# Kernel tuning notes

Measured on AMD Instinct MI355X. Metric: run time of the kernel, lower is better.

Reference implementation:

```python
import jax, jax.numpy as jnp
import numpy as np

LEAKY_ALPHA = 0.2  # TF default for tf.nn.leaky_relu


def setup_inputs() -> dict:
    key = jax.random.key(0)
    ks = jax.random.split(key, 5)
    B, N, F, O, H = 2, 4096, 256, 64, 4
    x = jax.random.normal(ks[0], (B, N, F), dtype=jnp.float32)
    bias = jax.random.normal(ks[1], (B, N, N), dtype=jnp.float32)
    W = jax.random.normal(ks[2], (H, F, O), dtype=jnp.float32) * (1.0 / np.sqrt(F))
    a = jax.random.normal(ks[3], (H, O), dtype=jnp.float32) * (1.0 / np.sqrt(O))
    b = jax.random.normal(ks[4], (H, O), dtype=jnp.float32) * 0.01
    return {"x": x, "bias": bias, "W": W, "a": a, "b": b}


def reference(x, bias, W, a, b):
    # x: [B,N,F], bias: [B,N,N], W: [H,F,O], a: [H,O], b: [H,O]
    h = jnp.einsum('bnf,hfo->bhno', x, W)          # transformed inputs per head
    w = jnp.einsum('bhno,ho->bhn', h, a)           # scalar score per node
    scores = w[:, :, :, None] + w[:, :, None, :]   # [B,H,N,N]: w_i + w_j
    logits = jax.nn.leaky_relu(scores, LEAKY_ALPHA) + bias[:, None, :, :]
    coefs = jax.nn.softmax(logits, axis=3)
    heads = jnp.einsum('bhnm,bhmo->bhno', coefs, h) + b[None, :, None, :]
    return jnp.mean(heads, axis=1)                 # (1/H) * sum of heads -> [B,N,O]
```

## Files before the change

### kernel.cpp

```cpp
#include <hip/hip_runtime.h>
#include <hip/hip_bf16.h>


constexpr int Bc = 2, Nc = 4096, Fc = 256, Oc = 64, Hc = 4;
constexpr float ALPHA = 0.2f;
constexpr float LOG2E = 1.4426950408889634f;

constexpr int BSTR = 260;
constexpr int BBUF = 16 * BSTR;
constexpr int SMEMF = 2 * BBUF;
constexpr int SLOTF = 1088;

typedef __attribute__((ext_vector_type(8))) short bf16x8;
typedef __attribute__((ext_vector_type(4))) float f32x4;

static __device__ inline short f2bf(float x) {
    __hip_bfloat16 h = __float2bfloat16(x);
    return *reinterpret_cast<short*>(&h);
}

static __device__ inline unsigned int rnpack(float a, float b) {
    const unsigned int au = __float_as_uint(a) + 0x8000u;
    const unsigned int bu = __float_as_uint(b) + 0x8000u;
    return (au >> 16) | (bu & 0xffff0000u);
}

static __device__ inline int frag_off(int jt, int k, int lane, int t) {
    return jt * 4096 + k * 512 + lane * 8 + t;
}

static __device__ inline void bar_lgkm() {
    asm volatile("s_waitcnt lgkmcnt(0)" ::: "memory");
    __builtin_amdgcn_s_barrier();
}

__global__ __launch_bounds__(256) void k_h(const float* __restrict__ x,
                                           const float* __restrict__ W,
                                           const float* __restrict__ a,
                                           short* __restrict__ hTB,
                                           float* __restrict__ wout) {
    __shared__ float xs[64][132];
    const int nb = Nc / 64;
    const int blk = blockIdx.x;
    const int nt = blk % nb;
    const int bh = blk / nb;
    const int h = bh % Hc;
    const int b = bh / Hc;
    const int tid = threadIdx.x;
    const int o_id = tid & 15, n_id = tid >> 4;
    const int o0 = o_id * 4, n0 = n_id * 4;

    float acc[4][4] = {};

    for (int fs = 0; fs < Fc; fs += 128) {
#pragma unroll
        for (int it = 0; it < 8; ++it) {
            int idx = it * 256 + tid;
            int r = idx >> 5, c = idx & 31;
            const float4 v = *reinterpret_cast<const float4*>(
                &x[((size_t)(b * Nc + nt * 64 + r)) * Fc + fs + c * 4]);
            *reinterpret_cast<float4*>(&xs[r][c * 4]) = v;
        }
        __syncthreads();
        for (int f = 0; f < 128; ++f) {
            const float4 wv = *reinterpret_cast<const float4*>(
                &W[((size_t)(h * Fc + fs + f)) * Oc + o0]);
            float xv[4];
#pragma unroll
            for (int r = 0; r < 4; ++r) xv[r] = xs[n0 + r][f];
#pragma unroll
            for (int r = 0; r < 4; ++r) {
                acc[r][0] = __builtin_fmaf(xv[r], wv.x, acc[r][0]);
                acc[r][1] = __builtin_fmaf(xv[r], wv.y, acc[r][1]);
                acc[r][2] = __builtin_fmaf(xv[r], wv.z, acc[r][2]);
                acc[r][3] = __builtin_fmaf(xv[r], wv.w, acc[r][3]);
            }
        }
        __syncthreads();
    }

    const float4 av = *reinterpret_cast<const float4*>(&a[h * Oc + o0]);
    float part[4];
#pragma unroll
    for (int r = 0; r < 4; ++r) {
        part[r] = acc[r][0] * av.x + acc[r][1] * av.y + acc[r][2] * av.z +
                  acc[r][3] * av.w;
#pragma unroll
        for (int off = 1; off < 16; off <<= 1)
            part[r] += __shfl_xor(part[r], off, 64);
    }
    const int n_glob = nt * 64 + n0;
    if (o_id == 0) {
#pragma unroll
        for (int r = 0; r < 4; ++r)
            wout[((size_t)(b * Hc + h)) * Nc + n_glob + r] = part[r] * LOG2E;
    }
    const int sub = n0 >> 5;
    const int lg = (n0 >> 3) & 3;
    const int t0 = n0 & 7;
    short* base = hTB + ((size_t)(b * Hc + h)) * (Nc * Oc);
#pragma unroll
    for (int c = 0; c < 4; ++c) {
        const int o = o0 + c;
        const int of = o >> 4, li = o & 15;
        short4 v;
        v.x = f2bf(acc[0][c]);
        v.y = f2bf(acc[1][c]);
        v.z = f2bf(acc[2][c]);
        v.w = f2bf(acc[3][c]);
        *reinterpret_cast<short4*>(&base[frag_off(nt, of * 2 + sub, lg * 16 + li, t0)]) = v;
    }
}

__global__ __launch_bounds__(512, 2) void k_attn(
    const float* __restrict__ bias, const float* __restrict__ wrowL,
    const short* __restrict__ hTB, float* __restrict__ hps) {
    __shared__ float smem[SMEMF];

    const int blk = blockIdx.x;
    const int xcd = blk & 7;
    const int lin = blk >> 3;
    const int pair = lin & 1;
    const int tl = xcd * 64 + (lin >> 1);
    const int it = tl & 255;
    const int b = tl >> 8;
    const int i0 = it * 16;
    const int tid = threadIdx.x;
    const int w = tid >> 6;
    const int hd = pair * 2 + (w & 1);
    const int q = w >> 1;
    const int lane = tid & 63;
    const int li = lane & 15, lg = lane >> 4;
    const int jl0 = lg * 8;

    const float wiL = wrowL[((size_t)(b * Hc + hd)) * Nc + i0 + li];
    const float* __restrict__ wjb = &wrowL[((size_t)(b * Hc + hd)) * Nc];
    const short* __restrict__ fb =
        hTB + ((size_t)(b * Hc + hd)) * (Nc * Oc) + lane * 8;

    const int srow = tid >> 5, sc4 = (tid & 31) * 4;
    const float* __restrict__ ssrc =
        &bias[((size_t)(b * Nc + i0 + srow)) * Nc + sc4];
    float* const sdst = &smem[srow * BSTR + sc4];

    f32x4 acc[4] = {{0.f, 0.f, 0.f, 0.f},
                    {0.f, 0.f, 0.f, 0.f},
                    {0.f, 0.f, 0.f, 0.f},
                    {0.f, 0.f, 0.f, 0.f}};
    float l_run = 0.f;

    {
        const float4 t0 = *reinterpret_cast<const float4*>(ssrc);
        const float4 t1 = *reinterpret_cast<const float4*>(ssrc + 128);
        *reinterpret_cast<float4*>(sdst) = t0;
        *reinterpret_cast<float4*>(sdst + 128) = t1;
    }
    float4 pA0 = *reinterpret_cast<const float4*>(ssrc + 256);
    float4 pA1 = *reinterpret_cast<const float4*>(ssrc + 256 + 128);
    bar_lgkm();

#pragma unroll 1
    for (int st = 0; st < 16; ++st) {
        if (st + 1 < 16) {
            float* d = sdst + ((st + 1) & 1) * BBUF;
            *reinterpret_cast<float4*>(d) = pA0;
            *reinterpret_cast<float4*>(d + 128) = pA1;
        }
        if (st + 2 < 16) {
            const float* sp = ssrc + (size_t)(st + 2) * 256;
            pA0 = *reinterpret_cast<const float4*>(sp);
            pA1 = *reinterpret_cast<const float4*>(sp + 128);
        }

        const int jt = st * 4 + q;
        bf16x8 fr[8];
#pragma unroll
        for (int k = 0; k < 8; ++k)
            fr[k] = *reinterpret_cast<const bf16x8*>(fb + jt * 4096 + k * 512);
        const int j0 = st * 256 + q * 64;
        const float* bp = &smem[(st & 1) * BBUF + li * BSTR + q * 64 + jl0];
        const float4 b03 = *reinterpret_cast<const float4*>(bp);
        const float4 b47 = *reinterpret_cast<const float4*>(bp + 4);
        const float4 b8b = *reinterpret_cast<const float4*>(bp + 32);
        const float4 bcf = *reinterpret_cast<const float4*>(bp + 36);
        const float bb[16] = {b03.x, b03.y, b03.z, b03.w, b47.x, b47.y,
                              b47.z, b47.w, b8b.x, b8b.y, b8b.z, b8b.w,
                              bcf.x, bcf.y, bcf.z, bcf.w};
        float s[16];
#pragma unroll
        for (int u = 0; u < 4; ++u) {
            const int off = (u >> 1) * 32 + (u & 1) * 4;
            const float4 wv =
                *reinterpret_cast<const float4*>(&wjb[j0 + jl0 + off]);
            float v, lv;
            v = wiL + wv.x; lv = fmaxf(v, ALPHA * v);
            s[u * 4 + 0] = __builtin_amdgcn_exp2f(__builtin_fmaf(bb[u * 4 + 0], LOG2E, lv));
            v = wiL + wv.y; lv = fmaxf(v, ALPHA * v);
            s[u * 4 + 1] = __builtin_amdgcn_exp2f(__builtin_fmaf(bb[u * 4 + 1], LOG2E, lv));
            v = wiL + wv.z; lv = fmaxf(v, ALPHA * v);
            s[u * 4 + 2] = __builtin_amdgcn_exp2f(__builtin_fmaf(bb[u * 4 + 2], LOG2E, lv));
            v = wiL + wv.w; lv = fmaxf(v, ALPHA * v);
            s[u * 4 + 3] = __builtin_amdgcn_exp2f(__builtin_fmaf(bb[u * 4 + 3], LOG2E, lv));
        }
        const float ta = (s[0] + s[1]) + (s[2] + s[3]);
        const float tb = (s[4] + s[5]) + (s[6] + s[7]);
        const float tc = (s[8] + s[9]) + (s[10] + s[11]);
        const float td = (s[12] + s[13]) + (s[14] + s[15]);
        l_run += (ta + tb) + (tc + td);
        bf16x8 pa0, pa1;
        unsigned int* pw0 = reinterpret_cast<unsigned int*>(&pa0);
        unsigned int* pw1 = reinterpret_cast<unsigned int*>(&pa1);
#pragma unroll
        for (int k2 = 0; k2 < 4; ++k2) {
            pw0[k2] = rnpack(s[k2 * 2], s[k2 * 2 + 1]);
            pw1[k2] = rnpack(s[8 + k2 * 2], s[8 + k2 * 2 + 1]);
        }
        __builtin_amdgcn_s_setprio(1);
#pragma unroll
        for (int of = 0; of < 4; ++of) {
            acc[of] = __builtin_amdgcn_mfma_f32_16x16x32_bf16(pa0, fr[of * 2 + 0],
                                                              acc[of], 0, 0, 0);
            acc[of] = __builtin_amdgcn_mfma_f32_16x16x32_bf16(pa1, fr[of * 2 + 1],
                                                              acc[of], 0, 0, 0);
        }
        __builtin_amdgcn_s_setprio(0);
        bar_lgkm();
    }

    if (q) {
        float* base = smem + ((w & 1) * 3 + (q - 1)) * SLOTF;
#pragma unroll
        for (int of = 0; of < 4; ++of)
            *reinterpret_cast<f32x4*>(&base[of * 256 + lane * 4]) = acc[of];
        base[1024 + lane] = l_run;
    }
    __syncthreads();
    if (q == 0) {
#pragma unroll
        for (int s = 0; s < 3; ++s) {
            const float* base = smem + ((w & 1) * 3 + s) * SLOTF;
#pragma unroll
            for (int of = 0; of < 4; ++of) {
                const f32x4 p =
                    *reinterpret_cast<const f32x4*>(&base[of * 256 + lane * 4]);
                acc[of][0] += p[0];
                acc[of][1] += p[1];
                acc[of][2] += p[2];
                acc[of][3] += p[3];
            }
            l_run += base[1024 + lane];
        }
        float lrow = l_run + __shfl_xor(l_run, 16, 64);
        lrow += __shfl_xor(lrow, 32, 64);
        const float linv = 1.0f / lrow;
        float sc[4];
#pragma unroll
        for (int r = 0; r < 4; ++r) sc[r] = __shfl(linv, lg * 4 + r, 64);
        float* hp = hps + (((size_t)(b * Hc + hd)) * Nc + i0) * Oc;
#pragma unroll
        for (int of = 0; of < 4; ++of)
#pragma unroll
            for (int r = 0; r < 4; ++r)
                hp[(size_t)(lg * 4 + r) * Oc + of * 16 + li] = acc[of][r] * sc[r];
    }
}

__global__ __launch_bounds__(256) void k_out(const float* __restrict__ hps,
                                             const float* __restrict__ bvec,
                                             float* __restrict__ out) {
    const int e = blockIdx.x * 256 + threadIdx.x;
    const int col = e & 63;
    const int bn = e >> 6;
    const int b = bn >> 12;
    const size_t plane = (size_t)Nc * Oc;
    const size_t off = ((size_t)(b * Hc) * Nc + (bn & 4095)) * Oc + col;
    const float v = hps[off] + hps[off + plane] + hps[off + 2 * plane] +
                    hps[off + 3 * plane];
    const float bm = 0.25f * (bvec[col] + bvec[Oc + col] + bvec[2 * Oc + col] +
                              bvec[3 * Oc + col]);
    out[e] = 0.25f * v + bm;
}

extern "C" void kernel_launch(void* const* d_in, const int* in_sizes, int n_in,
                              void* d_out, int out_size, void* d_ws, size_t ws_size,
                              hipStream_t stream) {
    const float* x = (const float*)d_in[0];
    const float* bias = (const float*)d_in[1];
    const float* W = (const float*)d_in[2];
    const float* a = (const float*)d_in[3];
    const float* bvec = (const float*)d_in[4];
    float* out = (float*)d_out;

    char* ws = (char*)d_ws;
    short* hTB = (short*)ws;
    float* wbuf = (float*)(ws + (size_t)Bc * Hc * Oc * Nc * 2);
    float* hps = (float*)(ws + (size_t)Bc * Hc * Oc * Nc * 2 +
                          (size_t)Bc * Hc * Nc * 4);

    k_h<<<Bc * Hc * (Nc / 64), 256, 0, stream>>>(x, W, a, hTB, wbuf);
    k_attn<<<Bc * (Nc / 16) * (Hc / 2), 512, 0, stream>>>(bias, wbuf, hTB, hps);
    k_out<<<(Bc * Nc * Oc) / 256, 256, 0, stream>>>(hps, bvec, out);
}
```

Before: 98.24 us.

## Process all four heads per block and fuse head-mean output into attention kernel

Each attention block now covers all four heads for its 16-row tile, with two waves per head each handling half of the key chunks, in place of two heads split four ways. This halves the grid and means each block loads its bias tile once for all four heads instead of twice across two blocks. The per-head results are reduced in shared memory and averaged with the bias vector directly into the output, which removes the hps intermediate buffer and the separate k_out launch. The trade-off is fewer blocks (512) and more serial work per wave, which may reduce latency hiding.

```diff
diff --git a/kernel.cpp b/kernel.cpp
--- a/kernel.cpp
+++ b/kernel.cpp
@@ -114,21 +114,21 @@
 
 __global__ __launch_bounds__(512, 2) void k_attn(
     const float* __restrict__ bias, const float* __restrict__ wrowL,
-    const short* __restrict__ hTB, float* __restrict__ hps) {
+    const short* __restrict__ hTB, const float* __restrict__ bvec,
+    float* __restrict__ out) {
     __shared__ float smem[SMEMF];
 
     const int blk = blockIdx.x;
     const int xcd = blk & 7;
     const int lin = blk >> 3;
-    const int pair = lin & 1;
-    const int tl = xcd * 64 + (lin >> 1);
+    const int tl = xcd * 64 + lin;
     const int it = tl & 255;
     const int b = tl >> 8;
     const int i0 = it * 16;
     const int tid = threadIdx.x;
     const int w = tid >> 6;
-    const int hd = pair * 2 + (w & 1);
-    const int q = w >> 1;
+    const int hd = w & 3;
+    const int half = w >> 2;
     const int lane = tid & 63;
     const int li = lane & 15, lg = lane >> 4;
     const int jl0 = lg * 8;
@@ -172,113 +172,115 @@
             pA1 = *reinterpret_cast<const float4*>(sp + 128);
         }
 
-        const int jt = st * 4 + q;
-        bf16x8 fr[8];
-#pragma unroll
-        for (int k = 0; k < 8; ++k)
-            fr[k] = *reinterpret_cast<const bf16x8*>(fb + jt * 4096 + k * 512);
-        const int j0 = st * 256 + q * 64;
-        const float* bp = &smem[(st & 1) * BBUF + li * BSTR + q * 64 + jl0];
-        const float4 b03 = *reinterpret_cast<const float4*>(bp);
-        const float4 b47 = *reinterpret_cast<const float4*>(bp + 4);
-        const float4 b8b = *reinterpret_cast<const float4*>(bp + 32);
-        const float4 bcf = *reinterpret_cast<const float4*>(bp + 36);
-        const float bb[16] = {b03.x, b03.y, b03.z, b03.w, b47.x, b47.y,
-                              b47.z, b47.w, b8b.x, b8b.y, b8b.z, b8b.w,
-                              bcf.x, bcf.y, bcf.z, bcf.w};
-        float s[16];
-#pragma unroll
-        for (int u = 0; u < 4; ++u) {
-            const int off = (u >> 1) * 32 + (u & 1) * 4;
-            const float4 wv =
-                *reinterpret_cast<const float4*>(&wjb[j0 + jl0 + off]);
-            float v, lv;
-            v = wiL + wv.x; lv = fmaxf(v, ALPHA * v);
-            s[u * 4 + 0] = __builtin_amdgcn_exp2f(__builtin_fmaf(bb[u * 4 + 0], LOG2E, lv));
-            v = wiL + wv.y; lv = fmaxf(v, ALPHA * v);
-            s[u * 4 + 1] = __builtin_amdgcn_exp2f(__builtin_fmaf(bb[u * 4 + 1], LOG2E, lv));
-            v = wiL + wv.z; lv = fmaxf(v, ALPHA * v);
-            s[u * 4 + 2] = __builtin_amdgcn_exp2f(__builtin_fmaf(bb[u * 4 + 2], LOG2E, lv));
-            v = wiL + wv.w; lv = fmaxf(v, ALPHA * v);
-            s[u * 4 + 3] = __builtin_amdgcn_exp2f(__builtin_fmaf(bb[u * 4 + 3], LOG2E, lv));
-        }
-        const float ta = (s[0] + s[1]) + (s[2] + s[3]);
-        const float tb = (s[4] + s[5]) + (s[6] + s[7]);
-        const float tc = (s[8] + s[9]) + (s[10] + s[11]);
-        const float td = (s[12] + s[13]) + (s[14] + s[15]);
-        l_run += (ta + tb) + (tc + td);
-        bf16x8 pa0, pa1;
-        unsigned int* pw0 = reinterpret_cast<unsigned int*>(&pa0);
-        unsigned int* pw1 = reinterpret_cast<unsigned int*>(&pa1);
-#pragma unroll
-        for (int k2 = 0; k2 < 4; ++k2) {
-            pw0[k2] = rnpack(s[k2 * 2], s[k2 * 2 + 1]);
-            pw1[k2] = rnpack(s[8 + k2 * 2], s[8 + k2 * 2 + 1]);
-        }
-        __builtin_amdgcn_s_setprio(1);
-#pragma unroll
-        for (int of = 0; of < 4; ++of) {
-            acc[of] = __builtin_amdgcn_mfma_f32_16x16x32_bf16(pa0, fr[of * 2 + 0],
-                                                              acc[of], 0, 0, 0);
-            acc[of] = __builtin_amdgcn_mfma_f32_16x16x32_bf16(pa1, fr[of * 2 + 1],
-                                                              acc[of], 0, 0, 0);
-        }
-        __builtin_amdgcn_s_setprio(0);
+#pragma unroll
+        for (int c = 0; c < 2; ++c) {
+            const int jc = half * 2 + c;
+            const int jt = st * 4 + jc;
+            const int j0 = st * 256 + jc * 64;
+            bf16x8 fr[8];
+#pragma unroll
+            for (int k = 0; k < 8; ++k)
+                fr[k] = *reinterpret_cast<const bf16x8*>(fb + jt * 4096 + k * 512);
+            const float* bp = &smem[(st & 1) * BBUF + li * BSTR + jc * 64 + jl0];
+            const float4 b03 = *reinterpret_cast<const float4*>(bp);
+            const float4 b47 = *reinterpret_cast<const float4*>(bp + 4);
+            const float4 b8b = *reinterpret_cast<const float4*>(bp + 32);
+            const float4 bcf = *reinterpret_cast<const float4*>(bp + 36);
+            const float bb[16] = {b03.x, b03.y, b03.z, b03.w, b47.x, b47.y,
+                                  b47.z, b47.w, b8b.x, b8b.y, b8b.z, b8b.w,
+                                  bcf.x, bcf.y, bcf.z, bcf.w};
+            float s[16];
+#pragma unroll
+            for (int u = 0; u < 4; ++u) {
+                const int off = (u >> 1) * 32 + (u & 1) * 4;
+                const float4 wv =
+                    *reinterpret_cast<const float4*>(&wjb[j0 + jl0 + off]);
+                float v, lv;
+                v = wiL + wv.x; lv = fmaxf(v, ALPHA * v);
+                s[u * 4 + 0] = __builtin_amdgcn_exp2f(__builtin_fmaf(bb[u * 4 + 0], LOG2E, lv));
+                v = wiL + wv.y; lv = fmaxf(v, ALPHA * v);
+                s[u * 4 + 1] = __builtin_amdgcn_exp2f(__builtin_fmaf(bb[u * 4 + 1], LOG2E, lv));
+                v = wiL + wv.z; lv = fmaxf(v, ALPHA * v);
+                s[u * 4 + 2] = __builtin_amdgcn_exp2f(__builtin_fmaf(bb[u * 4 + 2], LOG2E, lv));
+                v = wiL + wv.w; lv = fmaxf(v, ALPHA * v);
+                s[u * 4 + 3] = __builtin_amdgcn_exp2f(__builtin_fmaf(bb[u * 4 + 3], LOG2E, lv));
+            }
+            const float ta = (s[0] + s[1]) + (s[2] + s[3]);
+            const float tb = (s[4] + s[5]) + (s[6] + s[7]);
+            const float tc = (s[8] + s[9]) + (s[10] + s[11]);
+            const float td = (s[12] + s[13]) + (s[14] + s[15]);
+            l_run += (ta + tb) + (tc + td);
+            bf16x8 pa0, pa1;
+            unsigned int* pw0 = reinterpret_cast<unsigned int*>(&pa0);
+            unsigned int* pw1 = reinterpret_cast<unsigned int*>(&pa1);
+#pragma unroll
+            for (int k2 = 0; k2 < 4; ++k2) {
+                pw0[k2] = rnpack(s[k2 * 2], s[k2 * 2 + 1]);
+                pw1[k2] = rnpack(s[8 + k2 * 2], s[8 + k2 * 2 + 1]);
+            }
+            __builtin_amdgcn_s_setprio(1);
+#pragma unroll
+            for (int of = 0; of < 4; ++of) {
+                acc[of] = __builtin_amdgcn_mfma_f32_16x16x32_bf16(
+                    pa0, fr[of * 2 + 0], acc[of], 0, 0, 0);
+                acc[of] = __builtin_amdgcn_mfma_f32_16x16x32_bf16(
+                    pa1, fr[of * 2 + 1], acc[of], 0, 0, 0);
+            }
+            __builtin_amdgcn_s_setprio(0);
+        }
         bar_lgkm();
     }
 
-    if (q) {
-        float* base = smem + ((w & 1) * 3 + (q - 1)) * SLOTF;
+    if (half) {
+        float* base = smem + hd * SLOTF;
 #pragma unroll
         for (int of = 0; of < 4; ++of)
             *reinterpret_cast<f32x4*>(&base[of * 256 + lane * 4]) = acc[of];
         base[1024 + lane] = l_run;
     }
     __syncthreads();
-    if (q == 0) {
-#pragma unroll
-        for (int s = 0; s < 3; ++s) {
-            const float* base = smem + ((w & 1) * 3 + s) * SLOTF;
-#pragma unroll
-            for (int of = 0; of < 4; ++of) {
-                const f32x4 p =
-                    *reinterpret_cast<const f32x4*>(&base[of * 256 + lane * 4]);
-                acc[of][0] += p[0];
-                acc[of][1] += p[1];
-                acc[of][2] += p[2];
-                acc[of][3] += p[3];
-            }
-            l_run += base[1024 + lane];
-        }
+    if (!half) {
+        float* base = smem + hd * SLOTF;
+#pragma unroll
+        for (int of = 0; of < 4; ++of) {
+            const f32x4 p =
+                *reinterpret_cast<const f32x4*>(&base[of * 256 + lane * 4]);
+            acc[of][0] += p[0];
+            acc[of][1] += p[1];
+            acc[of][2] += p[2];
+            acc[of][3] += p[3];
+        }
+        l_run += base[1024 + lane];
         float lrow = l_run + __shfl_xor(l_run, 16, 64);
         lrow += __shfl_xor(lrow, 32, 64);
         const float linv = 1.0f / lrow;
         float sc[4];
 #pragma unroll
         for (int r = 0; r < 4; ++r) sc[r] = __shfl(linv, lg * 4 + r, 64);
-        float* hp = hps + (((size_t)(b * Hc + hd)) * Nc + i0) * Oc;
-#pragma unroll
-        for (int of = 0; of < 4; ++of)
-#pragma unroll
-            for (int r = 0; r < 4; ++r)
-                hp[(size_t)(lg * 4 + r) * Oc + of * 16 + li] = acc[of][r] * sc[r];
-    }
-}
-
-__global__ __launch_bounds__(256) void k_out(const float* __restrict__ hps,
-                                             const float* __restrict__ bvec,
-                                             float* __restrict__ out) {
-    const int e = blockIdx.x * 256 + threadIdx.x;
-    const int col = e & 63;
-    const int bn = e >> 6;
-    const int b = bn >> 12;
-    const size_t plane = (size_t)Nc * Oc;
-    const size_t off = ((size_t)(b * Hc) * Nc + (bn & 4095)) * Oc + col;
-    const float v = hps[off] + hps[off + plane] + hps[off + 2 * plane] +
-                    hps[off + 3 * plane];
-    const float bm = 0.25f * (bvec[col] + bvec[Oc + col] + bvec[2 * Oc + col] +
-                              bvec[3 * Oc + col]);
-    out[e] = 0.25f * v + bm;
+#pragma unroll
+        for (int of = 0; of < 4; ++of) {
+            f32x4 nv;
+            nv[0] = acc[of][0] * sc[0];
+            nv[1] = acc[of][1] * sc[1];
+            nv[2] = acc[of][2] * sc[2];
+            nv[3] = acc[of][3] * sc[3];
+            *reinterpret_cast<f32x4*>(&base[of * 256 + lane * 4]) = nv;
+        }
+    }
+    __syncthreads();
+#pragma unroll
+    for (int k = 0; k < 2; ++k) {
+        const int e = k * 512 + tid;
+        const int row = e >> 6, col = e & 63;
+        const int ofo = col >> 4, lio = col & 15, lgo = row >> 2, ro = row & 3;
+        const int eoff = ofo * 256 + (lgo * 16 + lio) * 4 + ro;
+        float osum = 0.f;
+#pragma unroll
+        for (int h = 0; h < 4; ++h) osum += smem[h * SLOTF + eoff];
+        const float bm = 0.25f * (bvec[col] + bvec[Oc + col] +
+                                  bvec[2 * Oc + col] + bvec[3 * Oc + col]);
+        out[((size_t)(b * Nc + i0 + row)) * Oc + col] = 0.25f * osum + bm;
+    }
 }
 
 extern "C" void kernel_launch(void* const* d_in, const int* in_sizes, int n_in,
@@ -294,10 +296,7 @@
     char* ws = (char*)d_ws;
     short* hTB = (short*)ws;
     float* wbuf = (float*)(ws + (size_t)Bc * Hc * Oc * Nc * 2);
-    float* hps = (float*)(ws + (size_t)Bc * Hc * Oc * Nc * 2 +
-                          (size_t)Bc * Hc * Nc * 4);
 
     k_h<<<Bc * Hc * (Nc / 64), 256, 0, stream>>>(x, W, a, hTB, wbuf);
-    k_attn<<<Bc * (Nc / 16) * (Hc / 2), 512, 0, stream>>>(bias, wbuf, hTB, hps);
-    k_out<<<(Bc * Nc * Oc) / 256, 256, 0, stream>>>(hps, bvec, out);
-}
+    k_attn<<<Bc * (Nc / 16), 512, 0, stream>>>(bias, wbuf, hTB, bvec, out);
+}
```

New measurement: 102.6 us. 4.5% more time.

## Split attention output columns across two wave groups with 1024-thread blocks

Applied to the files above, without the earlier changes.

Doubles the attention block to 1024 threads and splits the 64 output columns between two halves of the waves, so each wave holds two accumulators and loads four B fragments instead of eight. The bias tile staging is spread over more threads, with one float4 per thread per stage. This lowers per-wave register use so more waves can hide latency. The cost is that the softmax exponentials and score computation are now done twice, once in each output half, and there is more reduction traffic through shared memory. The launch bound of 1024 threads with 8 blocks is also an aggressive occupancy request.

```diff
diff --git a/kernel.cpp b/kernel.cpp
--- a/kernel.cpp
+++ b/kernel.cpp
@@ -9,7 +9,7 @@
 constexpr int BSTR = 260;
 constexpr int BBUF = 16 * BSTR;
 constexpr int SMEMF = 2 * BBUF;
-constexpr int SLOTF = 1088;
+constexpr int PSLOT = 576;
 
 typedef __attribute__((ext_vector_type(8))) short bf16x8;
 typedef __attribute__((ext_vector_type(4))) float f32x4;
@@ -112,7 +112,7 @@
     }
 }
 
-__global__ __launch_bounds__(512, 2) void k_attn(
+__global__ __launch_bounds__(1024, 8) void k_attn(
     const float* __restrict__ bias, const float* __restrict__ wrowL,
     const short* __restrict__ hTB, float* __restrict__ hps) {
     __shared__ float smem[SMEMF];
@@ -128,7 +128,8 @@
     const int tid = threadIdx.x;
     const int w = tid >> 6;
     const int hd = pair * 2 + (w & 1);
-    const int q = w >> 1;
+    const int q = (w >> 1) & 3;
+    const int oh = w >> 3;
     const int lane = tid & 63;
     const int li = lane & 15, lg = lane >> 4;
     const int jl0 = lg * 8;
@@ -136,47 +137,34 @@
     const float wiL = wrowL[((size_t)(b * Hc + hd)) * Nc + i0 + li];
     const float* __restrict__ wjb = &wrowL[((size_t)(b * Hc + hd)) * Nc];
     const short* __restrict__ fb =
-        hTB + ((size_t)(b * Hc + hd)) * (Nc * Oc) + lane * 8;
-
-    const int srow = tid >> 5, sc4 = (tid & 31) * 4;
+        hTB + ((size_t)(b * Hc + hd)) * (Nc * Oc) + oh * 4 * 512 + lane * 8;
+
+    const int srow = tid >> 6, sc4 = tid & 63;
     const float* __restrict__ ssrc =
-        &bias[((size_t)(b * Nc + i0 + srow)) * Nc + sc4];
-    float* const sdst = &smem[srow * BSTR + sc4];
-
-    f32x4 acc[4] = {{0.f, 0.f, 0.f, 0.f},
-                    {0.f, 0.f, 0.f, 0.f},
-                    {0.f, 0.f, 0.f, 0.f},
-                    {0.f, 0.f, 0.f, 0.f}};
+        &bias[((size_t)(b * Nc + i0 + srow)) * Nc + sc4 * 4];
+    float* const sdst = &smem[srow * BSTR + sc4 * 4];
+
+    f32x4 acc0 = {0.f, 0.f, 0.f, 0.f};
+    f32x4 acc1 = {0.f, 0.f, 0.f, 0.f};
     float l_run = 0.f;
 
-    {
-        const float4 t0 = *reinterpret_cast<const float4*>(ssrc);
-        const float4 t1 = *reinterpret_cast<const float4*>(ssrc + 128);
-        *reinterpret_cast<float4*>(sdst) = t0;
-        *reinterpret_cast<float4*>(sdst + 128) = t1;
-    }
-    float4 pA0 = *reinterpret_cast<const float4*>(ssrc + 256);
-    float4 pA1 = *reinterpret_cast<const float4*>(ssrc + 256 + 128);
+    *reinterpret_cast<float4*>(sdst) = *reinterpret_cast<const float4*>(ssrc);
+    float4 pA = *reinterpret_cast<const float4*>(ssrc + 256);
     bar_lgkm();
 
 #pragma unroll 1
     for (int st = 0; st < 16; ++st) {
-        if (st + 1 < 16) {
-            float* d = sdst + ((st + 1) & 1) * BBUF;
-            *reinterpret_cast<float4*>(d) = pA0;
-            *reinterpret_cast<float4*>(d + 128) = pA1;
-        }
-        if (st + 2 < 16) {
-            const float* sp = ssrc + (size_t)(st + 2) * 256;
-            pA0 = *reinterpret_cast<const float4*>(sp);
-            pA1 = *reinterpret_cast<const float4*>(sp + 128);
-        }
+        if (st + 1 < 16)
+            *reinterpret_cast<float4*>(sdst + ((st + 1) & 1) * BBUF) = pA;
+        if (st + 2 < 16)
+            pA = *reinterpret_cast<const float4*>(ssrc + (size_t)(st + 2) * 256);
 
         const int jt = st * 4 + q;
-        bf16x8 fr[8];
-#pragma unroll
-        for (int k = 0; k < 8; ++k)
-            fr[k] = *reinterpret_cast<const bf16x8*>(fb + jt * 4096 + k * 512);
+        const short* fp = fb + jt * 4096;
+        const bf16x8 fr0 = *reinterpret_cast<const bf16x8*>(fp);
+        const bf16x8 fr1 = *reinterpret_cast<const bf16x8*>(fp + 512);
+        const bf16x8 fr2 = *reinterpret_cast<const bf16x8*>(fp + 1024);
+        const bf16x8 fr3 = *reinterpret_cast<const bf16x8*>(fp + 1536);
         const int j0 = st * 256 + q * 64;
         const float* bp = &smem[(st & 1) * BBUF + li * BSTR + q * 64 + jl0];
         const float4 b03 = *reinterpret_cast<const float4*>(bp);
@@ -216,39 +204,34 @@
             pw1[k2] = rnpack(s[8 + k2 * 2], s[8 + k2 * 2 + 1]);
         }
         __builtin_amdgcn_s_setprio(1);
-#pragma unroll
-        for (int of = 0; of < 4; ++of) {
-            acc[of] = __builtin_amdgcn_mfma_f32_16x16x32_bf16(pa0, fr[of * 2 + 0],
-                                                              acc[of], 0, 0, 0);
-            acc[of] = __builtin_amdgcn_mfma_f32_16x16x32_bf16(pa1, fr[of * 2 + 1],
-                                                              acc[of], 0, 0, 0);
-        }
+        acc0 = __builtin_amdgcn_mfma_f32_16x16x32_bf16(pa0, fr0, acc0, 0, 0, 0);
+        acc0 = __builtin_amdgcn_mfma_f32_16x16x32_bf16(pa1, fr1, acc0, 0, 0, 0);
+        acc1 = __builtin_amdgcn_mfma_f32_16x16x32_bf16(pa0, fr2, acc1, 0, 0, 0);
+        acc1 = __builtin_amdgcn_mfma_f32_16x16x32_bf16(pa1, fr3, acc1, 0, 0, 0);
         __builtin_amdgcn_s_setprio(0);
         bar_lgkm();
     }
 
+    const int slotBase = (w & 1) * 6 + oh * 3;
     if (q) {
-        float* base = smem + ((w & 1) * 3 + (q - 1)) * SLOTF;
-#pragma unroll
-        for (int of = 0; of < 4; ++of)
-            *reinterpret_cast<f32x4*>(&base[of * 256 + lane * 4]) = acc[of];
-        base[1024 + lane] = l_run;
+        float* base = smem + (slotBase + q - 1) * PSLOT;
+        *reinterpret_cast<f32x4*>(&base[lane * 4]) = acc0;
+        *reinterpret_cast<f32x4*>(&base[256 + lane * 4]) = acc1;
+        base[512 + lane] = l_run;
     }
     __syncthreads();
     if (q == 0) {
 #pragma unroll
         for (int s = 0; s < 3; ++s) {
-            const float* base = smem + ((w & 1) * 3 + s) * SLOTF;
-#pragma unroll
-            for (int of = 0; of < 4; ++of) {
-                const f32x4 p =
-                    *reinterpret_cast<const f32x4*>(&base[of * 256 + lane * 4]);
-                acc[of][0] += p[0];
-                acc[of][1] += p[1];
-                acc[of][2] += p[2];
-                acc[of][3] += p[3];
-            }
-            l_run += base[1024 + lane];
+            const float* base = smem + (slotBase + s) * PSLOT;
+            const f32x4 p0 = *reinterpret_cast<const f32x4*>(&base[lane * 4]);
+            const f32x4 p1 =
+                *reinterpret_cast<const f32x4*>(&base[256 + lane * 4]);
+            acc0[0] += p0[0]; acc0[1] += p0[1];
+            acc0[2] += p0[2]; acc0[3] += p0[3];
+            acc1[0] += p1[0]; acc1[1] += p1[1];
+            acc1[2] += p1[2]; acc1[3] += p1[3];
+            l_run += base[512 + lane];
         }
         float lrow = l_run + __shfl_xor(l_run, 16, 64);
         lrow += __shfl_xor(lrow, 32, 64);
@@ -257,11 +240,12 @@
 #pragma unroll
         for (int r = 0; r < 4; ++r) sc[r] = __shfl(linv, lg * 4 + r, 64);
         float* hp = hps + (((size_t)(b * Hc + hd)) * Nc + i0) * Oc;
-#pragma unroll
-        for (int of = 0; of < 4; ++of)
-#pragma unroll
-            for (int r = 0; r < 4; ++r)
-                hp[(size_t)(lg * 4 + r) * Oc + of * 16 + li] = acc[of][r] * sc[r];
+        const int of0 = oh * 2, of1 = oh * 2 + 1;
+#pragma unroll
+        for (int r = 0; r < 4; ++r) {
+            hp[(size_t)(lg * 4 + r) * Oc + of0 * 16 + li] = acc0[r] * sc[r];
+            hp[(size_t)(lg * 4 + r) * Oc + of1 * 16 + li] = acc1[r] * sc[r];
+        }
     }
 }
 
@@ -298,6 +282,6 @@
                           (size_t)Bc * Hc * Nc * 4);
 
     k_h<<<Bc * Hc * (Nc / 64), 256, 0, stream>>>(x, W, a, hTB, wbuf);
-    k_attn<<<Bc * (Nc / 16) * (Hc / 2), 512, 0, stream>>>(bias, wbuf, hTB, hps);
+    k_attn<<<Bc * (Nc / 16) * (Hc / 2), 1024, 0, stream>>>(bias, wbuf, hTB, hps);
     k_out<<<(Bc * Nc * Oc) / 256, 256, 0, stream>>>(hps, bvec, out);
 }
```

After: 227.2 us. +131.3%, slower.

## Batch bias staging into four LDS buffers per barrier instead of double-buffered prefetch

Applied to the files above, without the earlier changes.

The bias tile staging changes from a double-buffered, two-stage register prefetch pipeline with a barrier every step to four batches. Each batch loads four 16x256 bias slices into four LDS buffers, syncs once, then runs four fully unrolled compute steps. This cuts the number of barriers and lets more global loads be in flight at once. In exchange the global bias loads no longer overlap with compute, LDS usage doubles (which may reduce occupancy), and the unrolled body increases register pressure.

```diff
diff --git a/kernel.cpp b/kernel.cpp
--- a/kernel.cpp
+++ b/kernel.cpp
@@ -8,7 +8,7 @@
 
 constexpr int BSTR = 260;
 constexpr int BBUF = 16 * BSTR;
-constexpr int SMEMF = 2 * BBUF;
+constexpr int SMEMF = 4 * BBUF;
 constexpr int SLOTF = 1088;
 
 typedef __attribute__((ext_vector_type(8))) short bf16x8;
@@ -149,84 +149,92 @@
                     {0.f, 0.f, 0.f, 0.f}};
     float l_run = 0.f;
 
-    {
-        const float4 t0 = *reinterpret_cast<const float4*>(ssrc);
-        const float4 t1 = *reinterpret_cast<const float4*>(ssrc + 128);
-        *reinterpret_cast<float4*>(sdst) = t0;
-        *reinterpret_cast<float4*>(sdst + 128) = t1;
-    }
-    float4 pA0 = *reinterpret_cast<const float4*>(ssrc + 256);
-    float4 pA1 = *reinterpret_cast<const float4*>(ssrc + 256 + 128);
-    bar_lgkm();
-
 #pragma unroll 1
-    for (int st = 0; st < 16; ++st) {
-        if (st + 1 < 16) {
-            float* d = sdst + ((st + 1) & 1) * BBUF;
-            *reinterpret_cast<float4*>(d) = pA0;
-            *reinterpret_cast<float4*>(d + 128) = pA1;
-        }
-        if (st + 2 < 16) {
-            const float* sp = ssrc + (size_t)(st + 2) * 256;
-            pA0 = *reinterpret_cast<const float4*>(sp);
-            pA1 = *reinterpret_cast<const float4*>(sp + 128);
-        }
-
-        const int jt = st * 4 + q;
-        bf16x8 fr[8];
-#pragma unroll
-        for (int k = 0; k < 8; ++k)
-            fr[k] = *reinterpret_cast<const bf16x8*>(fb + jt * 4096 + k * 512);
-        const int j0 = st * 256 + q * 64;
-        const float* bp = &smem[(st & 1) * BBUF + li * BSTR + q * 64 + jl0];
-        const float4 b03 = *reinterpret_cast<const float4*>(bp);
-        const float4 b47 = *reinterpret_cast<const float4*>(bp + 4);
-        const float4 b8b = *reinterpret_cast<const float4*>(bp + 32);
-        const float4 bcf = *reinterpret_cast<const float4*>(bp + 36);
-        const float bb[16] = {b03.x, b03.y, b03.z, b03.w, b47.x, b47.y,
-                              b47.z, b47.w, b8b.x, b8b.y, b8b.z, b8b.w,
-                              bcf.x, bcf.y, bcf.z, bcf.w};
-        float s[16];
-#pragma unroll
-        for (int u = 0; u < 4; ++u) {
-            const int off = (u >> 1) * 32 + (u & 1) * 4;
-            const float4 wv =
-                *reinterpret_cast<const float4*>(&wjb[j0 + jl0 + off]);
-            float v, lv;
-            v = wiL + wv.x; lv = fmaxf(v, ALPHA * v);
-            s[u * 4 + 0] = __builtin_amdgcn_exp2f(__builtin_fmaf(bb[u * 4 + 0], LOG2E, lv));
-            v = wiL + wv.y; lv = fmaxf(v, ALPHA * v);
-            s[u * 4 + 1] = __builtin_amdgcn_exp2f(__builtin_fmaf(bb[u * 4 + 1], LOG2E, lv));
-            v = wiL + wv.z; lv = fmaxf(v, ALPHA * v);
-            s[u * 4 + 2] = __builtin_amdgcn_exp2f(__builtin_fmaf(bb[u * 4 + 2], LOG2E, lv));
-            v = wiL + wv.w; lv = fmaxf(v, ALPHA * v);
-            s[u * 4 + 3] = __builtin_amdgcn_exp2f(__builtin_fmaf(bb[u * 4 + 3], LOG2E, lv));
-        }
-        const float ta = (s[0] + s[1]) + (s[2] + s[3]);
-        const float tb = (s[4] + s[5]) + (s[6] + s[7]);
-        const float tc = (s[8] + s[9]) + (s[10] + s[11]);
-        const float td = (s[12] + s[13]) + (s[14] + s[15]);
-        l_run += (ta + tb) + (tc + td);
-        bf16x8 pa0, pa1;
-        unsigned int* pw0 = reinterpret_cast<unsigned int*>(&pa0);
-        unsigned int* pw1 = reinterpret_cast<unsigned int*>(&pa1);
-#pragma unroll
-        for (int k2 = 0; k2 < 4; ++k2) {
-            pw0[k2] = rnpack(s[k2 * 2], s[k2 * 2 + 1]);
-            pw1[k2] = rnpack(s[8 + k2 * 2], s[8 + k2 * 2 + 1]);
-        }
-        __builtin_amdgcn_s_setprio(1);
-#pragma unroll
-        for (int of = 0; of < 4; ++of) {
-            acc[of] = __builtin_amdgcn_mfma_f32_16x16x32_bf16(pa0, fr[of * 2 + 0],
-                                                              acc[of], 0, 0, 0);
-            acc[of] = __builtin_amdgcn_mfma_f32_16x16x32_bf16(pa1, fr[of * 2 + 1],
-                                                              acc[of], 0, 0, 0);
-        }
-        __builtin_amdgcn_s_setprio(0);
+    for (int batch = 0; batch < 4; ++batch) {
+        if (batch) bar_lgkm();
+        {
+            const float* s0 = ssrc + (size_t)(batch * 4 + 0) * 256;
+            const float* s1 = ssrc + (size_t)(batch * 4 + 1) * 256;
+            const float* s2 = ssrc + (size_t)(batch * 4 + 2) * 256;
+            const float* s3 = ssrc + (size_t)(batch * 4 + 3) * 256;
+            const float4 a0 = *reinterpret_cast<const float4*>(s0);
+            const float4 b0 = *reinterpret_cast<const float4*>(s0 + 128);
+            const float4 a1 = *reinterpret_cast<const float4*>(s1);
+            const float4 b1 = *reinterpret_cast<const float4*>(s1 + 128);
+            const float4 a2 = *reinterpret_cast<const float4*>(s2);
+            const float4 b2 = *reinterpret_cast<const float4*>(s2 + 128);
+            const float4 a3 = *reinterpret_cast<const float4*>(s3);
+            const float4 b3 = *reinterpret_cast<const float4*>(s3 + 128);
+            *reinterpret_cast<float4*>(sdst + 0 * BBUF) = a0;
+            *reinterpret_cast<float4*>(sdst + 0 * BBUF + 128) = b0;
+            *reinterpret_cast<float4*>(sdst + 1 * BBUF) = a1;
+            *reinterpret_cast<float4*>(sdst + 1 * BBUF + 128) = b1;
+            *reinterpret_cast<float4*>(sdst + 2 * BBUF) = a2;
+            *reinterpret_cast<float4*>(sdst + 2 * BBUF + 128) = b2;
+            *reinterpret_cast<float4*>(sdst + 3 * BBUF) = a3;
+            *reinterpret_cast<float4*>(sdst + 3 * BBUF + 128) = b3;
+        }
         bar_lgkm();
-    }
-
+
+#pragma unroll
+        for (int k4 = 0; k4 < 4; ++k4) {
+            const int st = batch * 4 + k4;
+            const int jt = st * 4 + q;
+            bf16x8 fr[8];
+#pragma unroll
+            for (int k = 0; k < 8; ++k)
+                fr[k] = *reinterpret_cast<const bf16x8*>(fb + jt * 4096 + k * 512);
+            const int j0 = st * 256 + q * 64;
+            const float* bp = &smem[k4 * BBUF + li * BSTR + q * 64 + jl0];
+            const float4 b03 = *reinterpret_cast<const float4*>(bp);
+            const float4 b47 = *reinterpret_cast<const float4*>(bp + 4);
+            const float4 b8b = *reinterpret_cast<const float4*>(bp + 32);
+            const float4 bcf = *reinterpret_cast<const float4*>(bp + 36);
+            const float bb[16] = {b03.x, b03.y, b03.z, b03.w, b47.x, b47.y,
+                                  b47.z, b47.w, b8b.x, b8b.y, b8b.z, b8b.w,
+                                  bcf.x, bcf.y, bcf.z, bcf.w};
+            float s[16];
+#pragma unroll
+            for (int u = 0; u < 4; ++u) {
+                const int off = (u >> 1) * 32 + (u & 1) * 4;
+                const float4 wv =
+                    *reinterpret_cast<const float4*>(&wjb[j0 + jl0 + off]);
+                float v, lv;
+                v = wiL + wv.x; lv = fmaxf(v, ALPHA * v);
+                s[u * 4 + 0] = __builtin_amdgcn_exp2f(__builtin_fmaf(bb[u * 4 + 0], LOG2E, lv));
+                v = wiL + wv.y; lv = fmaxf(v, ALPHA * v);
+                s[u * 4 + 1] = __builtin_amdgcn_exp2f(__builtin_fmaf(bb[u * 4 + 1], LOG2E, lv));
+                v = wiL + wv.z; lv = fmaxf(v, ALPHA * v);
+                s[u * 4 + 2] = __builtin_amdgcn_exp2f(__builtin_fmaf(bb[u * 4 + 2], LOG2E, lv));
+                v = wiL + wv.w; lv = fmaxf(v, ALPHA * v);
+                s[u * 4 + 3] = __builtin_amdgcn_exp2f(__builtin_fmaf(bb[u * 4 + 3], LOG2E, lv));
+            }
+            const float ta = (s[0] + s[1]) + (s[2] + s[3]);
+            const float tb = (s[4] + s[5]) + (s[6] + s[7]);
+            const float tc = (s[8] + s[9]) + (s[10] + s[11]);
+            const float td = (s[12] + s[13]) + (s[14] + s[15]);
+            l_run += (ta + tb) + (tc + td);
+            bf16x8 pa0, pa1;
+            unsigned int* pw0 = reinterpret_cast<unsigned int*>(&pa0);
+            unsigned int* pw1 = reinterpret_cast<unsigned int*>(&pa1);
+#pragma unroll
+            for (int k2 = 0; k2 < 4; ++k2) {
+                pw0[k2] = rnpack(s[k2 * 2], s[k2 * 2 + 1]);
+                pw1[k2] = rnpack(s[8 + k2 * 2], s[8 + k2 * 2 + 1]);
+            }
+            __builtin_amdgcn_s_setprio(1);
+#pragma unroll
+            for (int of = 0; of < 4; ++of) {
+                acc[of] = __builtin_amdgcn_mfma_f32_16x16x32_bf16(
+                    pa0, fr[of * 2 + 0], acc[of], 0, 0, 0);
+                acc[of] = __builtin_amdgcn_mfma_f32_16x16x32_bf16(
+                    pa1, fr[of * 2 + 1], acc[of], 0, 0, 0);
+            }
+            __builtin_amdgcn_s_setprio(0);
+        }
+    }
+
+    __syncthreads();
     if (q) {
         float* base = smem + ((w & 1) * 3 + (q - 1)) * SLOTF;
 #pragma unroll
```

Result: slower. 119.0 us, median of 3 (+21.1%).
